# Optimization experiments

Hardware: AMD Instinct MI355X
Metric: run time of the kernel (lower is better)

## Reference

```python
import jax, jax.numpy as jnp
import numpy as np

N_NODES = 100000
N_USERS = 60000
N_MOVIES = 40000
N_EDGES = 1200000
D_IN = 64
D_EMB = 64


def setup_inputs() -> dict:
    key = jax.random.key(0)
    ks = jax.random.split(key, 6)
    x = jax.random.normal(ks[0], (N_NODES, D_IN), dtype=jnp.float32)
    edge_index = jax.random.randint(ks[1], (2, N_EDGES), 0, N_NODES, dtype=jnp.int64)
    # Glorot-ish init for the two GCNConv linear weights
    W1 = jax.random.normal(ks[2], (D_IN, D_EMB), dtype=jnp.float32) * (1.0 / np.sqrt(D_IN))
    b1 = jnp.zeros((D_EMB,), dtype=jnp.float32)
    W2 = jax.random.normal(ks[3], (D_EMB, D_EMB), dtype=jnp.float32) * (1.0 / np.sqrt(D_EMB))
    b2 = jnp.zeros((D_EMB,), dtype=jnp.float32)
    return {"x": x, "edge_index": edge_index, "W1": W1, "b1": b1, "W2": W2, "b2": b2}


def gcn_conv(x, W, b, src, dst):
    """PyG GCNConv: D^{-1/2}(A+I)D^{-1/2} X W + b with symmetric norm and self-loops."""
    h = x @ W  # [N, D_out]
    ones = jnp.ones(src.shape[0], dtype=h.dtype)
    # degree includes self-loop (+1)
    deg = jax.ops.segment_sum(ones, dst, num_segments=N_NODES) + 1.0
    dinv = jax.lax.rsqrt(deg)  # [N]
    coef = dinv[src] * dinv[dst]  # [E]
    agg = jax.ops.segment_sum(h[src] * coef[:, None], dst, num_segments=N_NODES)
    # self-loop contribution: norm = dinv[i]^2
    return agg + h * (dinv * dinv)[:, None] + b


def reference(x, edge_index, W1, b1, W2, b2):
    src, dst = edge_index[0], edge_index[1]
    h = gcn_conv(x, W1, b1, src, dst)
    h = jax.nn.relu(h)  # dropout is identity in eval mode
    h = gcn_conv(h, W2, b2, src, dst)
    user = h[:N_USERS]
    movie = h[N_USERS:N_USERS + N_MOVIES]
    return user, movie, h
```

## Files before the change

kernel.cpp:

```cpp
#include <hip/hip_runtime.h>

#define NN 100000
#define NE 1200000
#define DD 64
#define NPART 8
#define PSZ (NN / NPART)
#define EPB 4096
#define NCHUNK ((NE + EPB - 1) / EPB)
#define SCH 1024
#define SNB ((NN + SCH - 1) / SCH)

#define KCH3 96
#define CEH3 (NE / KCH3)
#define P3 2
#define BINS3 (NN / P3)
#define BINW3 (BINS3 / 4)

static __device__ __forceinline__ unsigned short f2bf(float f) {
    unsigned int u = __float_as_uint(f);
    u += 0x7fffu + ((u >> 16) & 1u);
    return (unsigned short)(u >> 16);
}
static __device__ __forceinline__ float bf_lo(unsigned int u) {
    return __uint_as_float(u << 16);
}
static __device__ __forceinline__ float bf_hi(unsigned int u) {
    return __uint_as_float(u & 0xffff0000u);
}

__global__ __launch_bounds__(1024) void k_hist3(const int* __restrict__ dst,
                                                unsigned char* __restrict__ H,
                                                unsigned char* __restrict__ rank8) {
    __shared__ unsigned int bins[BINW3];
    int k = blockIdx.x >> 1;
    int p = blockIdx.x & 1;
    int t = threadIdx.x;
    for (int i = t; i < BINW3; i += 1024) bins[i] = 0u;
    __syncthreads();
    int lo = p * BINS3;
    int beg = k * CEH3;
    for (int e4 = beg + t * 4; e4 < beg + CEH3; e4 += 4096) {
        int4 d4 = *(const int4*)&dst[e4];
        int dd[4] = {d4.x, d4.y, d4.z, d4.w};
#pragma unroll
        for (int j = 0; j < 4; ++j) {
            unsigned int r = (unsigned int)(dd[j] - lo);
            if (r < (unsigned int)BINS3) {
                unsigned int sh = (r & 3u) << 3;
                unsigned int old = atomicAdd(&bins[r >> 2], 1u << sh);
                rank8[e4 + j] = (unsigned char)((old >> sh) & 0xffu);
            }
        }
    }
    __syncthreads();
    unsigned int* Hw = (unsigned int*)(H + (size_t)k * NN + lo);
    for (int i = t; i < BINW3; i += 1024) Hw[i] = bins[i];
}

__global__ __launch_bounds__(256) void k_chunkscan3(unsigned int* __restrict__ H32,
                                                    int* __restrict__ degi) {
    int wd = blockIdx.x * 256 + threadIdx.x;
    if (wd >= NN / 4) return;
    unsigned int s = 0;
#pragma unroll 4
    for (int k = 0; k < KCH3; ++k) {
        size_t idx = (size_t)k * (NN / 4) + wd;
        unsigned int v = H32[idx];
        H32[idx] = s;
        s += v;
    }
    int4 dg;
    dg.x = (int)(s & 0xffu);
    dg.y = (int)((s >> 8) & 0xffu);
    dg.z = (int)((s >> 16) & 0xffu);
    dg.w = (int)(s >> 24);
    *(int4*)&degi[4 * wd] = dg;
}

__global__ __launch_bounds__(256) void k_fill3(const int* __restrict__ src,
                                               const int* __restrict__ dst,
                                               const unsigned char* __restrict__ rank8,
                                               const unsigned char* __restrict__ H,
                                               const int* __restrict__ rowptr,
                                               int* __restrict__ csr) {
    int e4 = (blockIdx.x * 256 + threadIdx.x) * 4;
    if (e4 >= NE) return;
    int4 d4 = *(const int4*)&dst[e4];
    int4 s4 = *(const int4*)&src[e4];
    unsigned int r4 = *(const unsigned int*)&rank8[e4];
    int dd[4] = {d4.x, d4.y, d4.z, d4.w};
    int ss[4] = {s4.x, s4.y, s4.z, s4.w};
#pragma unroll
    for (int j = 0; j < 4; ++j) {
        int e = e4 + j;
        int k = e / CEH3;
        int d = dd[j];
        int base = rowptr[d] + (int)H[(size_t)k * NN + d];
        csr[base + (int)((r4 >> (8 * j)) & 0xffu)] = ss[j];
    }
}

__global__ void k_hist_rank(const int* __restrict__ dst, int* __restrict__ degi,
                            int* __restrict__ rank, int ne) {
    int i = blockIdx.x * blockDim.x + threadIdx.x;
    if (i < ne) rank[i] = atomicAdd(&degi[dst[i]], 1);
}

__global__ __launch_bounds__(256) void k_hist(const int* __restrict__ dst,
                                              int* __restrict__ degi, int ne) {
    int part = blockIdx.x & (NPART - 1);
    int lo = part * PSZ, hi = lo + PSZ;
    int beg = (blockIdx.x >> 3) * EPB;
    int end = min(beg + EPB, ne);
    for (int e = beg + (int)threadIdx.x; e < end; e += 256) {
        int d = dst[e];
        if (d >= lo && d < hi) atomicAdd(&degi[d], 1);
    }
}

__global__ __launch_bounds__(256) void k_scan_local(const int* __restrict__ degi,
                                                    int* __restrict__ rowptr,
                                                    int* __restrict__ part,
                                                    float* __restrict__ dinv) {
    __shared__ int wsum[4];
    int t = threadIdx.x;
    int idx = blockIdx.x * SCH + t * 4;
    int d0 = 0, d1 = 0, d2 = 0, d3 = 0;
    if (idx + 3 < NN) {
        int4 v = *(const int4*)&degi[idx];
        d0 = v.x; d1 = v.y; d2 = v.z; d3 = v.w;
        float4 dv;
        dv.x = rsqrtf((float)d0 + 1.0f);
        dv.y = rsqrtf((float)d1 + 1.0f);
        dv.z = rsqrtf((float)d2 + 1.0f);
        dv.w = rsqrtf((float)d3 + 1.0f);
        *(float4*)&dinv[idx] = dv;
    } else {
        if (idx     < NN) { d0 = degi[idx];     dinv[idx]     = rsqrtf((float)d0 + 1.0f); }
        if (idx + 1 < NN) { d1 = degi[idx + 1]; dinv[idx + 1] = rsqrtf((float)d1 + 1.0f); }
        if (idx + 2 < NN) { d2 = degi[idx + 2]; dinv[idx + 2] = rsqrtf((float)d2 + 1.0f); }
        if (idx + 3 < NN) { d3 = degi[idx + 3]; dinv[idx + 3] = rsqrtf((float)d3 + 1.0f); }
    }
    int s = d0 + d1 + d2 + d3;
    int lane = t & 63;
    int incl = s;
#pragma unroll
    for (int off = 1; off < 64; off <<= 1) {
        int v = __shfl_up(incl, off);
        if (lane >= off) incl += v;
    }
    int wv = t >> 6;
    if (lane == 63) wsum[wv] = incl;
    __syncthreads();
    int woff = 0;
#pragma unroll
    for (int i = 0; i < 4; ++i) if (i < wv) woff += wsum[i];
    int excl = woff + incl - s;
    if (idx     < NN) rowptr[idx]     = excl;
    if (idx + 1 < NN) rowptr[idx + 1] = excl + d0;
    if (idx + 2 < NN) rowptr[idx + 2] = excl + d0 + d1;
    if (idx + 3 < NN) rowptr[idx + 3] = excl + d0 + d1 + d2;
    if (t == 255) part[blockIdx.x] = woff + incl;
}

__global__ __launch_bounds__(128) void k_scan_part(int* __restrict__ part) {
    __shared__ int sm[128];
    int t = threadIdx.x;
    int v = (t < SNB) ? part[t] : 0;
    sm[t] = v;
    __syncthreads();
    for (int off = 1; off < 128; off <<= 1) {
        int add = (t >= off) ? sm[t - off] : 0;
        __syncthreads();
        sm[t] += add;
        __syncthreads();
    }
    if (t < SNB) part[t] = sm[t] - v;
}

__global__ void k_scan_add(int* __restrict__ rowptr, const int* __restrict__ part) {
    int i = blockIdx.x * blockDim.x + threadIdx.x;
    if (i < NN) rowptr[i] += part[i >> 10];
    if (i == 0) rowptr[NN] = NE;
}

__global__ void k_fill_rank(const int* __restrict__ src, const int* __restrict__ dst,
                            const int* __restrict__ rank, const int* __restrict__ rowptr,
                            int* __restrict__ csr_src, int ne) {
    int e = blockIdx.x * blockDim.x + threadIdx.x;
    if (e < ne) csr_src[rowptr[dst[e]] + rank[e]] = src[e];
}

__global__ __launch_bounds__(256) void k_fill(const int* __restrict__ src,
                                              const int* __restrict__ dst,
                                              const int* __restrict__ rowptr,
                                              int* __restrict__ cnt,
                                              int* __restrict__ csr_src, int ne) {
    int part = blockIdx.x & (NPART - 1);
    int lo = part * PSZ, hi = lo + PSZ;
    int beg = (blockIdx.x >> 3) * EPB;
    int end = min(beg + EPB, ne);
    for (int e = beg + (int)threadIdx.x; e < end; e += 256) {
        int d = dst[e];
        if (d >= lo && d < hi) {
            int pos = rowptr[d] + atomicAdd(&cnt[d], 1);
            csr_src[pos] = src[e];
        }
    }
}

__global__ __launch_bounds__(256) void k_gemm_bf(const float* __restrict__ X,
                                                 const float* __restrict__ W,
                                                 unsigned short* __restrict__ Hb,
                                                 int nrows) {
    __shared__ float4 Ws4[64][16];
    __shared__ float  Xs[64][68];
    int tid = threadIdx.x;
    const float4* W4 = (const float4*)W;
    for (int i = tid; i < 64 * 16; i += 256) Ws4[i >> 4][i & 15] = W4[i];
    int row0 = blockIdx.x * 64;
    const float4* X4 = (const float4*)X;
    for (int i = tid; i < 64 * 16; i += 256) {
        int r = i >> 4, q = i & 15;
        int row = row0 + r;
        float4 v = make_float4(0.f, 0.f, 0.f, 0.f);
        if (row < nrows) v = X4[row * 16 + q];
        *((float4*)&Xs[r][q * 4]) = v;
    }
    __syncthreads();
    int c4 = tid & 15;
    int rg = tid >> 4;
    float4 acc0 = make_float4(0.f, 0.f, 0.f, 0.f);
    float4 acc1 = acc0, acc2 = acc0, acc3 = acc0;
#pragma unroll 4
    for (int k = 0; k < 64; ++k) {
        float4 w = Ws4[k][c4];
        float x0 = Xs[rg * 4 + 0][k];
        float x1 = Xs[rg * 4 + 1][k];
        float x2 = Xs[rg * 4 + 2][k];
        float x3 = Xs[rg * 4 + 3][k];
        acc0.x += x0 * w.x; acc0.y += x0 * w.y; acc0.z += x0 * w.z; acc0.w += x0 * w.w;
        acc1.x += x1 * w.x; acc1.y += x1 * w.y; acc1.z += x1 * w.z; acc1.w += x1 * w.w;
        acc2.x += x2 * w.x; acc2.y += x2 * w.y; acc2.z += x2 * w.z; acc2.w += x2 * w.w;
        acc3.x += x3 * w.x; acc3.y += x3 * w.y; acc3.z += x3 * w.z; acc3.w += x3 * w.w;
    }
    float4 accs[4] = {acc0, acc1, acc2, acc3};
#pragma unroll
    for (int i = 0; i < 4; ++i) {
        int row = row0 + rg * 4 + i;
        if (row < nrows) {
            ushort4 o;
            o.x = f2bf(accs[i].x); o.y = f2bf(accs[i].y);
            o.z = f2bf(accs[i].z); o.w = f2bf(accs[i].w);
            *((ushort4*)&Hb[row * 64 + c4 * 4]) = o;
        }
    }
}

__global__ __launch_bounds__(256) void k_reduce(const unsigned short* __restrict__ Hb,
                                                const int* __restrict__ rowptr,
                                                const int* __restrict__ csr_src,
                                                const float* __restrict__ dinv,
                                                const float* __restrict__ b,
                                                float* __restrict__ out0,
                                                float* __restrict__ out1,
                                                int do_relu) {
    int n = blockIdx.x * 4 + (threadIdx.x >> 6);
    if (n >= NN) return;
    int lane = threadIdx.x & 63;
    int eg = lane >> 3;
    int cg = lane & 7;
    float din = dinv[n];
    float acc[8];
#pragma unroll
    for (int j = 0; j < 8; ++j) acc[j] = 0.f;

    int e = rowptr[n], end = rowptr[n + 1];
    int idx = e + eg;
    bool v = idx < end;
    int s = v ? csr_src[idx] : 0;
    float cf = v ? dinv[s] * din : 0.f;

    while (e < end) {
        uint4 u = *(const uint4*)(Hb + (size_t)s * 64 + cg * 8);
        int e2 = e + 8;
        int idx2 = e2 + eg;
        bool v2 = idx2 < end;
        int s2 = v2 ? csr_src[idx2] : 0;
        float cf2 = v2 ? dinv[s2] * din : 0.f;
        acc[0] += bf_lo(u.x) * cf;  acc[1] += bf_hi(u.x) * cf;
        acc[2] += bf_lo(u.y) * cf;  acc[3] += bf_hi(u.y) * cf;
        acc[4] += bf_lo(u.z) * cf;  acc[5] += bf_hi(u.z) * cf;
        acc[6] += bf_lo(u.w) * cf;  acc[7] += bf_hi(u.w) * cf;
        s = s2; cf = cf2; e = e2;
    }

#pragma unroll
    for (int j = 0; j < 8; ++j) {
        acc[j] += __shfl_xor(acc[j], 8);
        acc[j] += __shfl_xor(acc[j], 16);
        acc[j] += __shfl_xor(acc[j], 32);
    }

    if (lane < 8) {
        uint4 us = *(const uint4*)(Hb + (size_t)n * 64 + cg * 8);
        float dd = din * din;
        float4 b0 = *(const float4*)(b + cg * 8);
        float4 b1 = *(const float4*)(b + cg * 8 + 4);
        float4 o0, o1;
        o0.x = acc[0] + bf_lo(us.x) * dd + b0.x;
        o0.y = acc[1] + bf_hi(us.x) * dd + b0.y;
        o0.z = acc[2] + bf_lo(us.y) * dd + b0.z;
        o0.w = acc[3] + bf_hi(us.y) * dd + b0.w;
        o1.x = acc[4] + bf_lo(us.z) * dd + b1.x;
        o1.y = acc[5] + bf_hi(us.z) * dd + b1.y;
        o1.z = acc[6] + bf_lo(us.w) * dd + b1.z;
        o1.w = acc[7] + bf_hi(us.w) * dd + b1.w;
        if (do_relu) {
            o0.x = fmaxf(o0.x, 0.f); o0.y = fmaxf(o0.y, 0.f);
            o0.z = fmaxf(o0.z, 0.f); o0.w = fmaxf(o0.w, 0.f);
            o1.x = fmaxf(o1.x, 0.f); o1.y = fmaxf(o1.y, 0.f);
            o1.z = fmaxf(o1.z, 0.f); o1.w = fmaxf(o1.w, 0.f);
        }
        *(float4*)(out0 + (size_t)n * 64 + cg * 8)     = o0;
        *(float4*)(out0 + (size_t)n * 64 + cg * 8 + 4) = o1;
        if (out1) {
            *(float4*)(out1 + (size_t)n * 64 + cg * 8)     = o0;
            *(float4*)(out1 + (size_t)n * 64 + cg * 8 + 4) = o1;
        }
    }
}

__global__ void k_copy4(const float4* __restrict__ in, float4* __restrict__ out, int n4) {
    int i = blockIdx.x * blockDim.x + threadIdx.x;
    if (i < n4) out[i] = in[i];
}

extern "C" void kernel_launch(void* const* d_in, const int* in_sizes, int n_in,
                              void* d_out, int out_size, void* d_ws, size_t ws_size,
                              hipStream_t stream) {
    const float* x  = (const float*)d_in[0];
    const int*   ei = (const int*)d_in[1];
    const float* W1 = (const float*)d_in[2];
    const float* b1 = (const float*)d_in[3];
    const float* W2 = (const float*)d_in[4];
    const float* b2 = (const float*)d_in[5];
    const int* src = ei;
    const int* dst = ei + NE;

    float* A = (float*)d_out;
    float* B = (float*)d_out + (size_t)NN * DD;

    char* w = (char*)d_ws;
    size_t off = 0;
    auto alloc = [&](size_t bytes) { void* p = w + off; off += (bytes + 255) & ~(size_t)255; return p; };
    float* dinv   = (float*)alloc(NN * sizeof(float));
    int*   degi   = (int*)  alloc(NN * sizeof(int));
    int*   cnt    = (int*)  alloc(NN * sizeof(int));
    int*   rowptr = (int*)  alloc((NN + 1) * sizeof(int));
    int*   part   = (int*)  alloc(512 * sizeof(int));
    int*   csr    = (int*)  alloc(NE * sizeof(int));
    size_t off_common = off;
    void* uni = alloc((size_t)NN * DD * sizeof(unsigned short));
    size_t off_uni = off;
    size_t need_rank = off_common + (((size_t)NE * sizeof(int) + 255) & ~(size_t)255);

    bool new_path  = (ws_size >= off_uni);
    bool rank_path = !new_path && (ws_size >= need_rank);

    unsigned char* Hh    = (unsigned char*)uni;
    unsigned char* rank8 = (unsigned char*)uni + (size_t)KCH3 * NN;
    int*           rank  = (int*)uni;
    unsigned short* Bb   = new_path ? (unsigned short*)uni : (unsigned short*)B;
    bool bb_in_ws = new_path;

    if (new_path) {
        k_hist3<<<KCH3 * P3, 1024, 0, stream>>>(dst, Hh, rank8);
        k_chunkscan3<<<(NN / 4 + 255) / 256, 256, 0, stream>>>((unsigned int*)Hh, degi);
        k_scan_local<<<SNB, 256, 0, stream>>>(degi, rowptr, part, dinv);
        k_scan_part<<<1, 128, 0, stream>>>(part);
        k_scan_add<<<(NN + 255) / 256, 256, 0, stream>>>(rowptr, part);
        k_fill3<<<(NE / 4 + 255) / 256, 256, 0, stream>>>(src, dst, rank8, Hh, rowptr, csr);
    } else if (rank_path) {
        hipMemsetAsync(degi, 0, NN * sizeof(int), stream);
        k_hist_rank<<<(NE + 255) / 256, 256, 0, stream>>>(dst, degi, rank, NE);
        k_scan_local<<<SNB, 256, 0, stream>>>(degi, rowptr, part, dinv);
        k_scan_part<<<1, 128, 0, stream>>>(part);
        k_scan_add<<<(NN + 255) / 256, 256, 0, stream>>>(rowptr, part);
        k_fill_rank<<<(NE + 255) / 256, 256, 0, stream>>>(src, dst, rank, rowptr, csr, NE);
    } else {
        hipMemsetAsync(degi, 0, NN * sizeof(int), stream);
        hipMemsetAsync(cnt, 0, NN * sizeof(int), stream);
        k_hist<<<NCHUNK * NPART, 256, 0, stream>>>(dst, degi, NE);
        k_scan_local<<<SNB, 256, 0, stream>>>(degi, rowptr, part, dinv);
        k_scan_part<<<1, 128, 0, stream>>>(part);
        k_scan_add<<<(NN + 255) / 256, 256, 0, stream>>>(rowptr, part);
        k_fill<<<NCHUNK * NPART, 256, 0, stream>>>(src, dst, rowptr, cnt, csr, NE);
    }

    k_gemm_bf<<<(NN + 63) / 64, 256, 0, stream>>>(x, W1, Bb, NN);
    k_reduce<<<(NN + 3) / 4, 256, 0, stream>>>(Bb, rowptr, csr, dinv, b1, A, nullptr, 1);

    k_gemm_bf<<<(NN + 63) / 64, 256, 0, stream>>>(A, W2, Bb, NN);
    if (bb_in_ws) {
        k_reduce<<<(NN + 3) / 4, 256, 0, stream>>>(Bb, rowptr, csr, dinv, b2, A, B, 0);
    } else {
        k_reduce<<<(NN + 3) / 4, 256, 0, stream>>>(Bb, rowptr, csr, dinv, b2, A, nullptr, 0);
        k_copy4<<<(NN * DD / 4 + 255) / 256, 256, 0, stream>>>((const float4*)A, (float4*)B, NN * DD / 4);
    }
}
```

Before: 265.1 us.

## Split chunk scan into segmented sum+scan and deepen gather prefetch in reduce

Replaces the single-pass column scan over 96 histogram chunks with a two-kernel segmented scan: one kernel sums four segments in parallel, and the second rescans each segment with its prefix offset. The goal is more parallelism than the 98-block serial scan had. The reduce kernel now prefetches the next neighbor's feature row one iteration ahead and loads the self-row early, to hide gather latency. k_fill3 also hoists the chunk index computation out of its loop. The cost is an extra kernel launch and an extra read of the histogram, and the deeper prefetch raises register pressure in reduce.

After: 263.4 us. About the same (-0.6%).

```diff
diff --git a/kernel.cpp b/kernel.cpp
--- a/kernel.cpp
+++ b/kernel.cpp
@@ -15,6 +15,9 @@
 #define P3 2
 #define BINS3 (NN / P3)
 #define BINW3 (BINS3 / 4)
+#define KSEG 4
+#define KPS (KCH3 / KSEG)
+#define NW4 (NN / 4)
 
 static __device__ __forceinline__ unsigned short f2bf(float f) {
     unsigned int u = __float_as_uint(f);
@@ -57,24 +60,42 @@
     for (int i = t; i < BINW3; i += 1024) Hw[i] = bins[i];
 }
 
-__global__ __launch_bounds__(256) void k_chunkscan3(unsigned int* __restrict__ H32,
-                                                    int* __restrict__ degi) {
+__global__ __launch_bounds__(256) void k_cseg_sum(const unsigned int* __restrict__ H32,
+                                                  unsigned int* __restrict__ aux) {
     int wd = blockIdx.x * 256 + threadIdx.x;
-    if (wd >= NN / 4) return;
+    int seg = blockIdx.y;
+    if (wd >= NW4) return;
     unsigned int s = 0;
-#pragma unroll 4
-    for (int k = 0; k < KCH3; ++k) {
-        size_t idx = (size_t)k * (NN / 4) + wd;
+#pragma unroll
+    for (int k = 0; k < KPS; ++k)
+        s += H32[(size_t)(seg * KPS + k) * NW4 + wd];
+    aux[seg * NW4 + wd] = s;
+}
+
+__global__ __launch_bounds__(256) void k_cseg_scan(unsigned int* __restrict__ H32,
+                                                   const unsigned int* __restrict__ aux,
+                                                   int* __restrict__ degi) {
+    int wd = blockIdx.x * 256 + threadIdx.x;
+    int seg = blockIdx.y;
+    if (wd >= NW4) return;
+    unsigned int base = 0;
+    for (int i = 0; i < seg; ++i) base += aux[i * NW4 + wd];
+    unsigned int s = base;
+#pragma unroll
+    for (int k = 0; k < KPS; ++k) {
+        size_t idx = (size_t)(seg * KPS + k) * NW4 + wd;
         unsigned int v = H32[idx];
         H32[idx] = s;
         s += v;
     }
-    int4 dg;
-    dg.x = (int)(s & 0xffu);
-    dg.y = (int)((s >> 8) & 0xffu);
-    dg.z = (int)((s >> 16) & 0xffu);
-    dg.w = (int)(s >> 24);
-    *(int4*)&degi[4 * wd] = dg;
+    if (seg == KSEG - 1) {
+        int4 dg;
+        dg.x = (int)(s & 0xffu);
+        dg.y = (int)((s >> 8) & 0xffu);
+        dg.z = (int)((s >> 16) & 0xffu);
+        dg.w = (int)(s >> 24);
+        *(int4*)&degi[4 * wd] = dg;
+    }
 }
 
 __global__ __launch_bounds__(256) void k_fill3(const int* __restrict__ src,
@@ -90,10 +111,9 @@
     unsigned int r4 = *(const unsigned int*)&rank8[e4];
     int dd[4] = {d4.x, d4.y, d4.z, d4.w};
     int ss[4] = {s4.x, s4.y, s4.z, s4.w};
+    int k = e4 / CEH3;
 #pragma unroll
     for (int j = 0; j < 4; ++j) {
-        int e = e4 + j;
-        int k = e / CEH3;
         int d = dd[j];
         int base = rowptr[d] + (int)H[(size_t)k * NN + d];
         csr[base + (int)((r4 >> (8 * j)) & 0xffu)] = ss[j];
@@ -271,28 +291,36 @@
     int eg = lane >> 3;
     int cg = lane & 7;
     float din = dinv[n];
+    uint4 us = *(const uint4*)(Hb + (size_t)n * 64 + cg * 8);
     float acc[8];
 #pragma unroll
     for (int j = 0; j < 8; ++j) acc[j] = 0.f;
 
     int e = rowptr[n], end = rowptr[n + 1];
-    int idx = e + eg;
-    bool v = idx < end;
-    int s = v ? csr_src[idx] : 0;
-    float cf = v ? dinv[s] * din : 0.f;
-
+    int idx0 = e + eg;
+    bool v0 = idx0 < end;
+    int s0 = v0 ? csr_src[idx0] : 0;
+    float cf0 = v0 ? dinv[s0] * din : 0.f;
+    uint4 u0 = *(const uint4*)(Hb + (size_t)s0 * 64 + cg * 8);
+    int idx1 = e + 8 + eg;
+    bool v1 = idx1 < end;
+    int s1 = v1 ? csr_src[idx1] : 0;
+    float cf1 = v1 ? dinv[s1] * din : 0.f;
+
+#pragma unroll 2
     while (e < end) {
-        uint4 u = *(const uint4*)(Hb + (size_t)s * 64 + cg * 8);
-        int e2 = e + 8;
-        int idx2 = e2 + eg;
+        uint4 u1 = *(const uint4*)(Hb + (size_t)s1 * 64 + cg * 8);
+        int idx2 = e + 16 + eg;
         bool v2 = idx2 < end;
         int s2 = v2 ? csr_src[idx2] : 0;
         float cf2 = v2 ? dinv[s2] * din : 0.f;
-        acc[0] += bf_lo(u.x) * cf;  acc[1] += bf_hi(u.x) * cf;
-        acc[2] += bf_lo(u.y) * cf;  acc[3] += bf_hi(u.y) * cf;
-        acc[4] += bf_lo(u.z) * cf;  acc[5] += bf_hi(u.z) * cf;
-        acc[6] += bf_lo(u.w) * cf;  acc[7] += bf_hi(u.w) * cf;
-        s = s2; cf = cf2; e = e2;
+        acc[0] += bf_lo(u0.x) * cf0;  acc[1] += bf_hi(u0.x) * cf0;
+        acc[2] += bf_lo(u0.y) * cf0;  acc[3] += bf_hi(u0.y) * cf0;
+        acc[4] += bf_lo(u0.z) * cf0;  acc[5] += bf_hi(u0.z) * cf0;
+        acc[6] += bf_lo(u0.w) * cf0;  acc[7] += bf_hi(u0.w) * cf0;
+        u0 = u1; cf0 = cf1;
+        s1 = s2; cf1 = cf2;
+        e += 8;
     }
 
 #pragma unroll
@@ -303,7 +331,6 @@
     }
 
     if (lane < 8) {
-        uint4 us = *(const uint4*)(Hb + (size_t)n * 64 + cg * 8);
         float dd = din * din;
         float4 b0 = *(const float4*)(b + cg * 8);
         float4 b1 = *(const float4*)(b + cg * 8 + 4);
@@ -376,7 +403,9 @@
 
     if (new_path) {
         k_hist3<<<KCH3 * P3, 1024, 0, stream>>>(dst, Hh, rank8);
-        k_chunkscan3<<<(NN / 4 + 255) / 256, 256, 0, stream>>>((unsigned int*)Hh, degi);
+        dim3 cgrid((NW4 + 255) / 256, KSEG);
+        k_cseg_sum<<<cgrid, 256, 0, stream>>>((unsigned int*)Hh, (unsigned int*)cnt);
+        k_cseg_scan<<<cgrid, 256, 0, stream>>>((unsigned int*)Hh, (const unsigned int*)cnt, degi);
         k_scan_local<<<SNB, 256, 0, stream>>>(degi, rowptr, part, dinv);
         k_scan_part<<<1, 128, 0, stream>>>(part);
         k_scan_add<<<(NN + 255) / 256, 256, 0, stream>>>(rowptr, part);
```
